# Kernel tuning notes

Measured on AMD Instinct MI355X. Metric: run time of the kernel, lower is better.

Reference implementation:

```python
import jax, jax.numpy as jnp
import numpy as np

EPS_LN = 1e-5
EPS_NORM = 1e-12


def _layernorm(h, g, b):
    mu = jnp.mean(h, axis=-1, keepdims=True)
    var = jnp.mean((h - mu) ** 2, axis=-1, keepdims=True)
    return (h - mu) * jax.lax.rsqrt(var + EPS_LN) * g + b


def _l2norm(h):
    n = jnp.linalg.norm(h, axis=-1, keepdims=True)
    return h / jnp.maximum(n, EPS_NORM)


def setup_inputs() -> dict:
    key = jax.random.key(0)
    ks = jax.random.split(key, 6)
    B, S, D = 8, 4096, 1024
    A, C, dc = 16, 8, 64      # n_anchors, n_comp, d_comp
    apc = A // C              # anchors per compartment = 2
    x = jax.random.normal(ks[0], (B, S, D), jnp.float32)
    anchors = jax.random.normal(ks[1], (A, D), jnp.float32)  # normalized inside forward
    ln_g = jnp.ones((D,), jnp.float32)
    ln_b = jnp.zeros((D,), jnp.float32)
    W1 = jax.random.normal(ks[2], (C, apc, 2 * dc), jnp.float32) / np.sqrt(apc)
    b1 = jnp.zeros((C, 2 * dc), jnp.float32)
    W2 = jax.random.normal(ks[3], (C, 2 * dc, dc), jnp.float32) / np.sqrt(2 * dc)
    b2 = jnp.zeros((C, dc), jnp.float32)
    cg = jnp.ones((C, dc), jnp.float32)
    cb = jnp.zeros((C, dc), jnp.float32)
    Wp = jax.random.normal(ks[4], (C * dc, D), jnp.float32) / np.sqrt(C * dc)
    bp = jnp.zeros((D,), jnp.float32)
    gate = jnp.full((D,), -3.0, jnp.float32)  # gate_init = -3.0
    return dict(x=x, anchors=anchors, ln_g=ln_g, ln_b=ln_b, W1=W1, b1=b1,
                W2=W2, b2=b2, cg=cg, cb=cb, Wp=Wp, bp=bp, gate=gate)


def reference(x, anchors, ln_g, ln_b, W1, b1, W2, b2, cg, cb, Wp, bp, gate):
    B, S, D = x.shape
    C, apc, _ = W1.shape
    dc = W2.shape[-1]
    # LayerNorm then L2-normalize each token
    h = _l2norm(_layernorm(x.reshape(B * S, D), ln_g, ln_b))  # (N, D)
    a = _l2norm(anchors)                                      # (A, D)
    tri = 1.0 - h @ a.T                                       # (N, A)
    # asgn = arange(A) % C -> comp k reads columns [k, k+C, ...]
    g = tri.reshape(-1, apc, C)                               # g[:, j, k] = tri[:, j*C + k]
    u = jnp.einsum('nak,kae->nke', g, W1) + b1                # (N, C, 2*dc)
    u = jnp.square(jnp.maximum(u, 0.0))                       # squared ReLU
    y = jnp.einsum('nke,ked->nkd', u, W2) + b2                # (N, C, dc)
    y = _layernorm(y, cg, cb)                                 # per-comp LayerNorm over dc
    y = y.reshape(-1, C * dc)                                 # concat comps in order
    update = (y @ Wp + bp).reshape(B, S, D)
    return x + jax.nn.sigmoid(gate) * update
```

## Files before the change

kernel.cpp:

```cpp
#include <hip/hip_runtime.h>
#include <hip/hip_bf16.h>

#define DIM 1024
#define NANCH 16
#define NCOMP 8
#define DC 64
#define DC2 128
#define EPS_LN 1e-5f
#define EPS_NORM 1e-12f

typedef __bf16 bf16x8 __attribute__((ext_vector_type(8)));
typedef float f32x4 __attribute__((ext_vector_type(4)));

template <int CTRL>
__device__ __forceinline__ float rr_add(float v) {
  return v + __int_as_float(__builtin_amdgcn_update_dpp(
                 0, __float_as_int(v), CTRL, 0xF, 0xF, true));
}
__device__ __forceinline__ float rowsum16(float v) {
  v = rr_add<0x121>(v);
  v = rr_add<0x122>(v);
  v = rr_add<0x124>(v);
  v = rr_add<0x128>(v);
  return v;
}
__device__ __forceinline__ float wavesum64(float v) {
  v = rowsum16(v);
  v += __shfl_xor(v, 16);
  v += __shfl_xor(v, 32);
  return v;
}

__device__ __forceinline__ void gload16(const __hip_bfloat16* g, __hip_bfloat16* l) {
  __builtin_amdgcn_global_load_lds(
      (const __attribute__((address_space(1))) unsigned int*)g,
      (__attribute__((address_space(3))) unsigned int*)l, 16, 0, 0);
}

__global__ __launch_bounds__(256) void knorm_anchors(
    const float* __restrict__ anchors, float* __restrict__ An) {
  int a = blockIdx.x, t = threadIdx.x;
  int lane = t & 63, wid = t >> 6;
  __shared__ float red[4];
  float v[4]; float ss = 0.f;
#pragma unroll
  for (int i = 0; i < 4; i++) {
    v[i] = anchors[a * DIM + t + 256 * i];
    ss += v[i] * v[i];
  }
  for (int off = 32; off; off >>= 1) ss += __shfl_down(ss, off);
  if (lane == 0) red[wid] = ss;
  __syncthreads();
  float inv = 1.f / fmaxf(sqrtf(red[0] + red[1] + red[2] + red[3]), EPS_NORM);
#pragma unroll
  for (int i = 0; i < 4; i++) An[a * DIM + t + 256 * i] = v[i] * inv;
}

__global__ __launch_bounds__(256) void ktrans(
    const float* __restrict__ Wp, __hip_bfloat16* __restrict__ WpT) {
  __shared__ float tile[64][65];
  int bj = blockIdx.x, bk = blockIdx.y;
  int tx = threadIdx.x & 63, ty = threadIdx.x >> 6;
#pragma unroll
  for (int i = 0; i < 16; i++) {
    int r = ty + 4 * i;
    tile[r][tx] = Wp[(size_t)(bk * 64 + r) * DIM + bj * 64 + tx];
  }
  __syncthreads();
#pragma unroll
  for (int i = 0; i < 16; i++) {
    int r = ty + 4 * i;
    WpT[(size_t)(bj * 64 + r) * 512 + bk * 64 + tx] = __float2bfloat16(tile[tx][r]);
  }
}

__global__ __launch_bounds__(256) void kprep(
    const float* __restrict__ W2, const float* __restrict__ An,
    __hip_bfloat16* __restrict__ W2B, __hip_bfloat16* __restrict__ AnB) {
  int id = blockIdx.x * 256 + threadIdx.x;
  if (id < 65536) {
    int j = id & 7, lane = (id >> 3) & 63, ks = (id >> 9) & 3,
        nt = (id >> 11) & 3, k = id >> 13;
    int e = ks * 32 + (lane >> 4) * 8 + j;
    int n = nt * 16 + (lane & 15);
    W2B[id] = __float2bfloat16(W2[k * (DC2 * DC) + e * DC + n]);
  } else {
    int id2 = id - 65536;
    int j = id2 & 7, lane = (id2 >> 3) & 63, ks = id2 >> 9;
    int e = ks * 32 + (lane >> 4) * 8 + j;
    int a = lane & 15;
    AnB[id2] = __float2bfloat16(An[a * DIM + e]);
  }
}

#define LDA_H 1032
__global__ __launch_bounds__(256, 4) void ktoken(
    const float* __restrict__ x, const __hip_bfloat16* __restrict__ AnB,
    const float* __restrict__ ln_g, const float* __restrict__ ln_b,
    const float* __restrict__ W1, const float* __restrict__ b1,
    const __hip_bfloat16* __restrict__ W2B, const float* __restrict__ b2,
    const float* __restrict__ cg, const float* __restrict__ cb,
    __hip_bfloat16* __restrict__ yout) {
  int t = threadIdx.x;
  int lane = t & 63, w = t >> 6;
  int l15 = lane & 15, quad = lane >> 4;
  int n0 = blockIdx.x * 8;

  __shared__ __hip_bfloat16 hu[8 * LDA_H];
  __shared__ float tri_s[8 * 16];
  __shared__ float part[4 * 32 * 4];

  bf16x8 anb[8];
#pragma unroll
  for (int i = 0; i < 8; i++)
    anb[i] = *(const bf16x8*)(&AnB[(w * 8 + i) * 512 + lane * 8]);

  float gv[16], bv[16];
#pragma unroll
  for (int i = 0; i < 4; i++) {
    f32x4 g4 = *(const f32x4*)(&ln_g[i * 256 + lane * 4]);
    f32x4 b4 = *(const f32x4*)(&ln_b[i * 256 + lane * 4]);
#pragma unroll
    for (int j = 0; j < 4; j++) { gv[i * 4 + j] = g4[j]; bv[i * 4 + j] = b4[j]; }
  }
  f32x4 xv4[2][4];
#pragma unroll
  for (int it = 0; it < 2; it++) {
    const float* xr = x + (size_t)(n0 + w * 2 + it) * DIM;
#pragma unroll
    for (int i = 0; i < 4; i++)
      xv4[it][i] = *(const f32x4*)(&xr[i * 256 + lane * 4]);
  }
#pragma unroll
  for (int it = 0; it < 2; it++) {
    int tok = w * 2 + it;
    float xv[16], s = 0.f, s2 = 0.f;
#pragma unroll
    for (int i = 0; i < 4; i++) {
#pragma unroll
      for (int j = 0; j < 4; j++) {
        float v = xv4[it][i][j];
        xv[i * 4 + j] = v; s += v; s2 += v * v;
      }
    }
    s = wavesum64(s);
    s2 = wavesum64(s2);
    float mu = s * (1.f / DIM);
    float rstd = rsqrtf(s2 * (1.f / DIM) - mu * mu + EPS_LN);
    float ss = 0.f;
#pragma unroll
    for (int i = 0; i < 16; i++) {
      float h = (xv[i] - mu) * rstd * gv[i] + bv[i];
      xv[i] = h; ss += h * h;
    }
    ss = wavesum64(ss);
    float inv = 1.f / fmaxf(sqrtf(ss), EPS_NORM);
#pragma unroll
    for (int i = 0; i < 4; i++) {
      union { uint2 u; __hip_bfloat16 h[4]; } pk;
#pragma unroll
      for (int j = 0; j < 4; j++) pk.h[j] = __float2bfloat16(xv[i * 4 + j] * inv);
      *(uint2*)(&hu[tok * LDA_H + i * 256 + lane * 4]) = pk.u;
    }
  }
  __syncthreads();

  {
    f32x4 tacc = {0.f, 0.f, 0.f, 0.f};
    int ar = l15 & 7;
#pragma unroll
    for (int i = 0; i < 8; i++) {
      int ks = w * 8 + i;
      bf16x8 afr = *(const bf16x8*)(&hu[ar * LDA_H + ks * 32 + quad * 8]);
      tacc = __builtin_amdgcn_mfma_f32_16x16x32_bf16(afr, anb[i], tacc, 0, 0, 0);
    }
    if (quad < 2) *(f32x4*)(&part[(w * 32 + (lane & 31)) * 4]) = tacc;
  }
  __syncthreads();
  if (t < 128) {
    int ln = t & 31, rg = t >> 5;
    float v = part[(0 * 32 + ln) * 4 + rg] + part[(1 * 32 + ln) * 4 + rg] +
              part[(2 * 32 + ln) * 4 + rg] + part[(3 * 32 + ln) * 4 + rg];
    int m = (ln >> 4) * 4 + rg, a = ln & 15;
    tri_s[m * 16 + a] = 1.f - v;
  }

  bf16x8 bfv[16];
#pragma unroll
  for (int q = 0; q < 16; q++)
    bfv[q] = *(const bf16x8*)(&W2B[(size_t)((w * 2) * 16 + q) * 512 + lane * 8]);
  __syncthreads();

  {
    int k = t >> 5;
    int e0 = (t * 4) & 127;
    f32x4 w1a = *(const f32x4*)(&W1[k * 256 + e0]);
    f32x4 w1b = *(const f32x4*)(&W1[k * 256 + 128 + e0]);
    f32x4 b1v = *(const f32x4*)(&b1[k * 128 + e0]);
#pragma unroll
    for (int tok = 0; tok < 8; tok++) {
      float t0 = tri_s[tok * 16 + k], t1 = tri_s[tok * 16 + 8 + k];
      union { unsigned long long u; __hip_bfloat16 h[4]; } pk;
#pragma unroll
      for (int j = 0; j < 4; j++) {
        float uu = t0 * w1a[j] + t1 * w1b[j] + b1v[j];
        uu = fmaxf(uu, 0.f);
        pk.h[j] = __float2bfloat16(uu * uu);
      }
      *(unsigned long long*)(&hu[tok * LDA_H + t * 4]) = pk.u;
    }
  }
  __syncthreads();

#pragma unroll
  for (int kc = 0; kc < 2; kc++) {
    int k = w * 2 + kc;
    int ar = l15 & 7;
    bf16x8 afr[4];
#pragma unroll
    for (int ks = 0; ks < 4; ks++)
      afr[ks] = *(const bf16x8*)(&hu[ar * LDA_H + k * 128 + ks * 32 + quad * 8]);
    f32x4 acc[4] = {{0,0,0,0},{0,0,0,0},{0,0,0,0},{0,0,0,0}};
#pragma unroll
    for (int nt = 0; nt < 4; nt++) {
#pragma unroll
      for (int ks = 0; ks < 4; ks++)
        acc[nt] = __builtin_amdgcn_mfma_f32_16x16x32_bf16(afr[ks], bfv[nt * 4 + ks],
                                                          acc[nt], 0, 0, 0);
    }
    if (kc == 0) {
#pragma unroll
      for (int q = 0; q < 16; q++)
        bfv[q] = *(const bf16x8*)(&W2B[(size_t)((w * 2 + 1) * 16 + q) * 512 + lane * 8]);
    }
    float vals[4][4], s1[4] = {0,0,0,0}, s2[4] = {0,0,0,0};
#pragma unroll
    for (int nt = 0; nt < 4; nt++) {
      float b2v = b2[k * 64 + nt * 16 + l15];
#pragma unroll
      for (int r = 0; r < 4; r++) {
        float v = acc[nt][r] + b2v;
        vals[nt][r] = v; s1[r] += v; s2[r] += v * v;
      }
    }
#pragma unroll
    for (int r = 0; r < 4; r++) {
      s1[r] = rowsum16(s1[r]);
      s2[r] = rowsum16(s2[r]);
    }
#pragma unroll
    for (int r = 0; r < 4; r++) {
      float mu = s1[r] * (1.f / DC);
      float rs = rsqrtf(s2[r] * (1.f / DC) - mu * mu + EPS_LN);
      int tokrow = quad * 4 + r;
      if (tokrow < 8) {
#pragma unroll
        for (int nt = 0; nt < 4; nt++) {
          int d = nt * 16 + l15;
          float yn = (vals[nt][r] - mu) * rs * cg[k * 64 + d] + cb[k * 64 + d];
          yout[(size_t)(n0 + tokrow) * 512 + k * 64 + d] = __float2bfloat16(yn);
        }
      }
    }
  }
}

__global__ __launch_bounds__(256, 4) void kgemm(
    const __hip_bfloat16* __restrict__ Y, const __hip_bfloat16* __restrict__ WpT,
    const float* __restrict__ x, const float* __restrict__ bp,
    const float* __restrict__ gate, float* __restrict__ out) {
  __shared__ alignas(16) __hip_bfloat16 As[128 * 64];
  __shared__ alignas(16) __hip_bfloat16 Bs[128 * 64];
  int t = threadIdx.x, lane = t & 63, wid = t >> 6;
  int bm = blockIdx.x, bj = blockIdx.y;
  int wm = (wid >> 1) * 64, wj = (wid & 1) * 64;
  int l15 = lane & 15, quad = lane >> 4;

  f32x4 acc[4][4] = {};

  int srow[4], scol[4];
#pragma unroll
  for (int it = 0; it < 4; it++) {
    int byteo = it * 4096 + t * 16;
    int row = byteo >> 7, colb = byteo & 127;
    srow[it] = row;
    scol[it] = (colb ^ ((row & 7) << 4)) >> 1;
  }

  for (int kt = 0; kt < 8; kt++) {
    int k0 = kt * 64;
#pragma unroll
    for (int it = 0; it < 4; it++) {
      gload16(Y + (size_t)(bm * 128 + srow[it]) * 512 + k0 + scol[it],
              As + (it * 4096 + t * 16) / 2);
      gload16(WpT + (size_t)(bj * 128 + srow[it]) * 512 + k0 + scol[it],
              Bs + (it * 4096 + t * 16) / 2);
    }
    __syncthreads();
#pragma unroll
    for (int kk = 0; kk < 64; kk += 32) {
      bf16x8 af[4], bfr[4];
#pragma unroll
      for (int i = 0; i < 4; i++) {
        int ra = wm + i * 16 + l15, rb = wj + i * 16 + l15;
        int cb2 = (kk + quad * 8) * 2;
        af[i]  = *(const bf16x8*)((const char*)As + ra * 128 + (cb2 ^ ((ra & 7) << 4)));
        bfr[i] = *(const bf16x8*)((const char*)Bs + rb * 128 + (cb2 ^ ((rb & 7) << 4)));
      }
#pragma unroll
      for (int i = 0; i < 4; i++)
#pragma unroll
        for (int j = 0; j < 4; j++)
          acc[i][j] = __builtin_amdgcn_mfma_f32_16x16x32_bf16(af[i], bfr[j], acc[i][j], 0, 0, 0);
    }
    __syncthreads();
  }

  float sg[4], bpv[4];
#pragma unroll
  for (int j = 0; j < 4; j++) {
    int gc = bj * 128 + wj + j * 16 + l15;
    sg[j] = 1.f / (1.f + expf(-gate[gc]));
    bpv[j] = bp[gc];
  }
#pragma unroll
  for (int i = 0; i < 4; i++) {
#pragma unroll
    for (int j = 0; j < 4; j++) {
      int gc = bj * 128 + wj + j * 16 + l15;
#pragma unroll
      for (int r = 0; r < 4; r++) {
        int gr = bm * 128 + wm + i * 16 + quad * 4 + r;
        size_t idx = (size_t)gr * DIM + gc;
        out[idx] = x[idx] + sg[j] * (acc[i][j][r] + bpv[j]);
      }
    }
  }
}

extern "C" void kernel_launch(void* const* d_in, const int* in_sizes, int n_in,
                              void* d_out, int out_size, void* d_ws, size_t ws_size,
                              hipStream_t stream) {
  const float* x       = (const float*)d_in[0];
  const float* anchors = (const float*)d_in[1];
  const float* ln_g    = (const float*)d_in[2];
  const float* ln_b    = (const float*)d_in[3];
  const float* W1      = (const float*)d_in[4];
  const float* b1      = (const float*)d_in[5];
  const float* W2      = (const float*)d_in[6];
  const float* b2      = (const float*)d_in[7];
  const float* cg      = (const float*)d_in[8];
  const float* cb      = (const float*)d_in[9];
  const float* Wp      = (const float*)d_in[10];
  const float* bp      = (const float*)d_in[11];
  const float* gate    = (const float*)d_in[12];

  int N = in_sizes[0] / DIM;

  char* w = (char*)d_ws;
  size_t off = 0;
  float* An           = (float*)(w + off);           off += 64 << 10;
  __hip_bfloat16* WpT = (__hip_bfloat16*)(w + off);  off += 1 << 20;
  __hip_bfloat16* W2B = (__hip_bfloat16*)(w + off);  off += 128 << 10;
  __hip_bfloat16* AnB = (__hip_bfloat16*)(w + off);  off += 32 << 10;
  __hip_bfloat16* Yb  = (__hip_bfloat16*)(w + off);

  knorm_anchors<<<NANCH, 256, 0, stream>>>(anchors, An);
  ktrans<<<dim3(16, 8), 256, 0, stream>>>(Wp, WpT);
  kprep<<<320, 256, 0, stream>>>(W2, An, W2B, AnB);
  ktoken<<<N / 8, 256, 0, stream>>>(x, AnB, ln_g, ln_b, W1, b1, W2B, b2, cg, cb, Yb);
  kgemm<<<dim3(N / 128, DIM / 128), 256, 0, stream>>>(Yb, WpT, x, bp, gate,
                                                      (float*)d_out);
}
```

Measured before the change: 342.1 us.

## Merge weight-prep kernels and cut ktoken register pressure for higher occupancy

Three preprocessing kernels (anchor normalization, Wp transpose, W2/anchor repacking) are folded into one launch that uses block-index ranges, which removes two kernel launches and the intermediate An buffer. In ktoken, the anchor and W2 fragments are no longer preloaded into registers; they are loaded just before each MFMA, and x loads are moved inside the per-token loop. Launch bounds go from 4 to 7 blocks per SM so more waves can hide latency. The cost is that loads now sit directly on the MFMA critical path, with less prefetching to overlap them.

```diff
diff --git a/kernel.cpp b/kernel.cpp
--- a/kernel.cpp
+++ b/kernel.cpp
@@ -37,64 +37,62 @@
       (__attribute__((address_space(3))) unsigned int*)l, 16, 0, 0);
 }
 
-__global__ __launch_bounds__(256) void knorm_anchors(
-    const float* __restrict__ anchors, float* __restrict__ An) {
-  int a = blockIdx.x, t = threadIdx.x;
-  int lane = t & 63, wid = t >> 6;
-  __shared__ float red[4];
-  float v[4]; float ss = 0.f;
-#pragma unroll
-  for (int i = 0; i < 4; i++) {
-    v[i] = anchors[a * DIM + t + 256 * i];
-    ss += v[i] * v[i];
-  }
-  for (int off = 32; off; off >>= 1) ss += __shfl_down(ss, off);
-  if (lane == 0) red[wid] = ss;
-  __syncthreads();
-  float inv = 1.f / fmaxf(sqrtf(red[0] + red[1] + red[2] + red[3]), EPS_NORM);
-#pragma unroll
-  for (int i = 0; i < 4; i++) An[a * DIM + t + 256 * i] = v[i] * inv;
-}
-
-__global__ __launch_bounds__(256) void ktrans(
-    const float* __restrict__ Wp, __hip_bfloat16* __restrict__ WpT) {
-  __shared__ float tile[64][65];
-  int bj = blockIdx.x, bk = blockIdx.y;
-  int tx = threadIdx.x & 63, ty = threadIdx.x >> 6;
-#pragma unroll
-  for (int i = 0; i < 16; i++) {
-    int r = ty + 4 * i;
-    tile[r][tx] = Wp[(size_t)(bk * 64 + r) * DIM + bj * 64 + tx];
-  }
-  __syncthreads();
-#pragma unroll
-  for (int i = 0; i < 16; i++) {
-    int r = ty + 4 * i;
-    WpT[(size_t)(bj * 64 + r) * 512 + bk * 64 + tx] = __float2bfloat16(tile[tx][r]);
-  }
-}
-
-__global__ __launch_bounds__(256) void kprep(
-    const float* __restrict__ W2, const float* __restrict__ An,
+__global__ __launch_bounds__(256) void kprepall(
+    const float* __restrict__ anchors, const float* __restrict__ Wp,
+    const float* __restrict__ W2, __hip_bfloat16* __restrict__ WpT,
     __hip_bfloat16* __restrict__ W2B, __hip_bfloat16* __restrict__ AnB) {
-  int id = blockIdx.x * 256 + threadIdx.x;
-  if (id < 65536) {
+  __shared__ float smem[64 * 65 + 16];
+  int b = blockIdx.x, t = threadIdx.x;
+
+  if (b < 16) {
+    int a = b, lane = t & 63, wid = t >> 6;
+    float v[4]; float ss = 0.f;
+#pragma unroll
+    for (int i = 0; i < 4; i++) {
+      v[i] = anchors[a * DIM + t + 256 * i];
+      ss += v[i] * v[i];
+    }
+    for (int off = 32; off; off >>= 1) ss += __shfl_down(ss, off);
+    if (lane == 0) smem[4160 + wid] = ss;
+    __syncthreads();
+    float inv = 1.f / fmaxf(sqrtf(smem[4160] + smem[4161] + smem[4162] + smem[4163]),
+                            EPS_NORM);
+#pragma unroll
+    for (int i = 0; i < 4; i++) smem[t + 256 * i] = v[i] * inv;
+    __syncthreads();
+#pragma unroll
+    for (int q = 0; q < 4; q++) {
+      int idx = t * 4 + q;
+      int ks = idx >> 5, hi = (idx >> 3) & 3, j = idx & 7;
+      AnB[ks * 512 + (hi * 16 + a) * 8 + j] = __float2bfloat16(smem[idx]);
+    }
+  } else if (b < 144) {
+    int bidx = b - 16, bj = bidx & 15, bk = bidx >> 4;
+    int tx = t & 63, ty = t >> 6;
+#pragma unroll
+    for (int i = 0; i < 16; i++) {
+      int r = ty + 4 * i;
+      smem[r * 65 + tx] = Wp[(size_t)(bk * 64 + r) * DIM + bj * 64 + tx];
+    }
+    __syncthreads();
+#pragma unroll
+    for (int i = 0; i < 16; i++) {
+      int r = ty + 4 * i;
+      WpT[(size_t)(bj * 64 + r) * 512 + bk * 64 + tx] =
+          __float2bfloat16(smem[tx * 65 + r]);
+    }
+  } else {
+    int id = (b - 144) * 256 + t;
     int j = id & 7, lane = (id >> 3) & 63, ks = (id >> 9) & 3,
         nt = (id >> 11) & 3, k = id >> 13;
     int e = ks * 32 + (lane >> 4) * 8 + j;
     int n = nt * 16 + (lane & 15);
     W2B[id] = __float2bfloat16(W2[k * (DC2 * DC) + e * DC + n]);
-  } else {
-    int id2 = id - 65536;
-    int j = id2 & 7, lane = (id2 >> 3) & 63, ks = id2 >> 9;
-    int e = ks * 32 + (lane >> 4) * 8 + j;
-    int a = lane & 15;
-    AnB[id2] = __float2bfloat16(An[a * DIM + e]);
   }
 }
 
 #define LDA_H 1032
-__global__ __launch_bounds__(256, 4) void ktoken(
+__global__ __launch_bounds__(256, 7) void ktoken(
     const float* __restrict__ x, const __hip_bfloat16* __restrict__ AnB,
     const float* __restrict__ ln_g, const float* __restrict__ ln_b,
     const float* __restrict__ W1, const float* __restrict__ b1,
@@ -110,11 +108,6 @@
   __shared__ float tri_s[8 * 16];
   __shared__ float part[4 * 32 * 4];
 
-  bf16x8 anb[8];
-#pragma unroll
-  for (int i = 0; i < 8; i++)
-    anb[i] = *(const bf16x8*)(&AnB[(w * 8 + i) * 512 + lane * 8]);
-
   float gv[16], bv[16];
 #pragma unroll
   for (int i = 0; i < 4; i++) {
@@ -123,23 +116,17 @@
 #pragma unroll
     for (int j = 0; j < 4; j++) { gv[i * 4 + j] = g4[j]; bv[i * 4 + j] = b4[j]; }
   }
-  f32x4 xv4[2][4];
-#pragma unroll
-  for (int it = 0; it < 2; it++) {
-    const float* xr = x + (size_t)(n0 + w * 2 + it) * DIM;
-#pragma unroll
-    for (int i = 0; i < 4; i++)
-      xv4[it][i] = *(const f32x4*)(&xr[i * 256 + lane * 4]);
-  }
 #pragma unroll
   for (int it = 0; it < 2; it++) {
     int tok = w * 2 + it;
+    const float* xr = x + (size_t)(n0 + tok) * DIM;
     float xv[16], s = 0.f, s2 = 0.f;
 #pragma unroll
     for (int i = 0; i < 4; i++) {
+      f32x4 v4 = *(const f32x4*)(&xr[i * 256 + lane * 4]);
 #pragma unroll
       for (int j = 0; j < 4; j++) {
-        float v = xv4[it][i][j];
+        float v = v4[j];
         xv[i * 4 + j] = v; s += v; s2 += v * v;
       }
     }
@@ -169,10 +156,10 @@
     f32x4 tacc = {0.f, 0.f, 0.f, 0.f};
     int ar = l15 & 7;
 #pragma unroll
-    for (int i = 0; i < 8; i++) {
-      int ks = w * 8 + i;
+    for (int ks = w * 8; ks < w * 8 + 8; ks++) {
       bf16x8 afr = *(const bf16x8*)(&hu[ar * LDA_H + ks * 32 + quad * 8]);
-      tacc = __builtin_amdgcn_mfma_f32_16x16x32_bf16(afr, anb[i], tacc, 0, 0, 0);
+      bf16x8 bfr = *(const bf16x8*)(&AnB[ks * 512 + lane * 8]);
+      tacc = __builtin_amdgcn_mfma_f32_16x16x32_bf16(afr, bfr, tacc, 0, 0, 0);
     }
     if (quad < 2) *(f32x4*)(&part[(w * 32 + (lane & 31)) * 4]) = tacc;
   }
@@ -184,11 +171,6 @@
     int m = (ln >> 4) * 4 + rg, a = ln & 15;
     tri_s[m * 16 + a] = 1.f - v;
   }
-
-  bf16x8 bfv[16];
-#pragma unroll
-  for (int q = 0; q < 16; q++)
-    bfv[q] = *(const bf16x8*)(&W2B[(size_t)((w * 2) * 16 + q) * 512 + lane * 8]);
   __syncthreads();
 
   {
@@ -224,14 +206,10 @@
 #pragma unroll
     for (int nt = 0; nt < 4; nt++) {
 #pragma unroll
-      for (int ks = 0; ks < 4; ks++)
-        acc[nt] = __builtin_amdgcn_mfma_f32_16x16x32_bf16(afr[ks], bfv[nt * 4 + ks],
-                                                          acc[nt], 0, 0, 0);
-    }
-    if (kc == 0) {
-#pragma unroll
-      for (int q = 0; q < 16; q++)
-        bfv[q] = *(const bf16x8*)(&W2B[(size_t)((w * 2 + 1) * 16 + q) * 512 + lane * 8]);
+      for (int ks = 0; ks < 4; ks++) {
+        bf16x8 bfr = *(const bf16x8*)(&W2B[(size_t)(((k * 4 + nt) * 4 + ks)) * 512 + lane * 8]);
+        acc[nt] = __builtin_amdgcn_mfma_f32_16x16x32_bf16(afr[ks], bfr, acc[nt], 0, 0, 0);
+      }
     }
     float vals[4][4], s1[4] = {0,0,0,0}, s2[4] = {0,0,0,0};
 #pragma unroll
@@ -359,15 +337,12 @@
 
   char* w = (char*)d_ws;
   size_t off = 0;
-  float* An           = (float*)(w + off);           off += 64 << 10;
   __hip_bfloat16* WpT = (__hip_bfloat16*)(w + off);  off += 1 << 20;
   __hip_bfloat16* W2B = (__hip_bfloat16*)(w + off);  off += 128 << 10;
   __hip_bfloat16* AnB = (__hip_bfloat16*)(w + off);  off += 32 << 10;
   __hip_bfloat16* Yb  = (__hip_bfloat16*)(w + off);
 
-  knorm_anchors<<<NANCH, 256, 0, stream>>>(anchors, An);
-  ktrans<<<dim3(16, 8), 256, 0, stream>>>(Wp, WpT);
-  kprep<<<320, 256, 0, stream>>>(W2, An, W2B, AnB);
+  kprepall<<<400, 256, 0, stream>>>(anchors, Wp, W2, WpT, W2B, AnB);
   ktoken<<<N / 8, 256, 0, stream>>>(x, AnB, ln_g, ln_b, W1, b1, W2B, b2, cg, cb, Yb);
   kgemm<<<dim3(N / 128, DIM / 128), 256, 0, stream>>>(Yb, WpT, x, bp, gate,
                                                       (float*)d_out);
```

After: 340.9 us. About the same (-0.3%).
